# Kernel optimization log

Measured on AMD Instinct MI355X. Metric: run time of the kernel, lower is better.

Reference implementation:

```python
import jax, jax.numpy as jnp
import numpy as np

TEMPERATURE = 0.5
EPS = 1e-8  # torch F.cosine_similarity norm clamp
B, D = 4096, 768


def setup_inputs() -> dict:
    key = jax.random.key(0)
    k1, k2 = jax.random.split(key)
    return {
        "aug_hidden1": jax.random.normal(k1, (B, D), dtype=jnp.float32),
        "aug_hidden2": jax.random.normal(k2, (B, D), dtype=jnp.float32),
    }


def reference(aug_hidden1, aug_hidden2):
    b = aug_hidden1.shape[0]
    n = 2 * b
    h = jnp.concatenate([aug_hidden1, aug_hidden2], axis=0)  # [N, D]
    norm = jnp.maximum(jnp.linalg.norm(h, axis=1, keepdims=True), EPS)
    hn = h / norm
    # cosine-similarity matrix via GEMM (equivalent to broadcasted cosine_similarity)
    sim = jnp.matmul(hn, hn.T) / TEMPERATURE  # [N, N]
    idx = jnp.arange(n)
    pos = sim[idx, (idx + b) % n]  # positives: sim(i, i+B) and sim(i+B, i)
    # row logits = {positive} U {all entries except diagonal and pair} = all off-diagonal
    # entries, so CrossEntropy(label=0) == logsumexp(off-diagonal row) - positive
    sim_masked = jnp.where(jnp.eye(n, dtype=bool), -jnp.inf, sim)
    lse = jax.nn.logsumexp(sim_masked, axis=1)  # [N]
    return jnp.mean(lse - pos)
```

## Files before the change

kernel.cpp:

```cpp
#include <hip/hip_runtime.h>
#include <hip/hip_bf16.h>


#define B_SZ 4096
#define D_SZ 768
#define N_SZ 8192
#define ROWB 384
constexpr float INV_T = 2.0f;

typedef float f32x16 __attribute__((ext_vector_type(16)));
typedef int i32x8 __attribute__((ext_vector_type(8)));
typedef int i32x4 __attribute__((ext_vector_type(4)));
typedef __attribute__((address_space(1))) const unsigned int gu32;
typedef __attribute__((address_space(3))) unsigned int lu32;

__device__ inline void async16(const void* g, void* l) {
    __builtin_amdgcn_global_load_lds((gu32*)g, (lu32*)l, 16, 0, 0);
}

__device__ inline float hsum32_dpp(float x) {
    float s = x, t;
    t = __int_as_float(__builtin_amdgcn_update_dpp(0, __float_as_int(s), 0x111, 0xf, 0xf, true)); s += t;
    t = __int_as_float(__builtin_amdgcn_update_dpp(0, __float_as_int(s), 0x112, 0xf, 0xf, true)); s += t;
    t = __int_as_float(__builtin_amdgcn_update_dpp(0, __float_as_int(s), 0x114, 0xf, 0xf, true)); s += t;
    t = __int_as_float(__builtin_amdgcn_update_dpp(0, __float_as_int(s), 0x118, 0xf, 0xf, true)); s += t;
    t = __int_as_float(__builtin_amdgcn_update_dpp(0, __float_as_int(s), 0x142, 0xa, 0xf, true)); s += t;
    return s;
}

__device__ inline unsigned fp4_enc(float v) {
    float a = fabsf(v);
    unsigned c;
    if (a < 1.25f)      c = (a < 0.25f) ? 0u : (a < 0.75f) ? 1u : 2u;
    else if (a < 2.5f)  c = (a < 1.75f) ? 3u : 4u;
    else                c = (a < 3.5f) ? 5u : (a < 5.0f) ? 6u : 7u;
    return c | (v < 0.f ? 8u : 0u);
}

__global__ __launch_bounds__(256) void prep_k(const float* __restrict__ h1,
                                              const float* __restrict__ h2,
                                              unsigned char* __restrict__ hn4,
                                              float* __restrict__ pos,
                                              float* __restrict__ out) {
    if (blockIdx.x == 0 && threadIdx.x == 0) out[0] = 0.f;
    const int i = blockIdx.x * 4 + (threadIdx.x >> 6);
    const int lane = threadIdx.x & 63;
    const float4* a4 = (const float4*)(h1 + (size_t)i * D_SZ);
    const float4* b4 = (const float4*)(h2 + (size_t)i * D_SZ);
    float4 av[3], bv[3];
    float sa = 0.f, sb = 0.f, dt = 0.f;
#pragma unroll
    for (int j = 0; j < 3; ++j) {
        av[j] = a4[lane * 3 + j];
        bv[j] = b4[lane * 3 + j];
        sa += av[j].x * av[j].x + av[j].y * av[j].y + av[j].z * av[j].z + av[j].w * av[j].w;
        sb += bv[j].x * bv[j].x + bv[j].y * bv[j].y + bv[j].z * bv[j].z + bv[j].w * bv[j].w;
        dt += av[j].x * bv[j].x + av[j].y * bv[j].y + av[j].z * bv[j].z + av[j].w * bv[j].w;
    }
#pragma unroll
    for (int m = 1; m < 64; m <<= 1) {
        sa += __shfl_xor(sa, m, 64);
        sb += __shfl_xor(sb, m, 64);
        dt += __shfl_xor(dt, m, 64);
    }
    const float n1 = fmaxf(sqrtf(sa), 1e-8f), n2 = fmaxf(sqrtf(sb), 1e-8f);
    const float i1 = 1.0f / n1, i2 = 1.0f / n2;
    const float s1 = i1 * 16.0f, s2 = i2 * 16.0f;
    unsigned short* d1 = (unsigned short*)(hn4 + (size_t)i * ROWB);
    unsigned short* d2 = (unsigned short*)(hn4 + (size_t)(i + B_SZ) * ROWB);
#pragma unroll
    for (int j = 0; j < 3; ++j) {
        float va[4] = {av[j].x, av[j].y, av[j].z, av[j].w};
        float vb[4] = {bv[j].x, bv[j].y, bv[j].z, bv[j].w};
        unsigned u1 = 0, u2 = 0;
#pragma unroll
        for (int e = 0; e < 4; ++e) {
            u1 |= fp4_enc(va[e] * s1) << (4 * e);
            u2 |= fp4_enc(vb[e] * s2) << (4 * e);
        }
        d1[lane * 3 + j] = (unsigned short)u1;
        d2[lane * 3 + j] = (unsigned short)u2;
    }
    if (lane == 0) {
        float p = dt * i1 * i2 * INV_T;
        pos[i] = p;
        pos[i + B_SZ] = p;
    }
}

#define BM 128
#define SLAB 4096
#define WINB 64
#define NWIN 6
#define BUFS 8192

__global__ __launch_bounds__(512) void gemm_reduce_k(const unsigned char* __restrict__ hn4,
                                                     float* __restrict__ part) {
    __shared__ __align__(16) unsigned char As[3 * BUFS];
    __shared__ __align__(16) unsigned char Bs[3 * BUFS];
    const int b0 = blockIdx.x;
    const int b = (b0 & 7) * 260 + (b0 >> 3);
    int tx = (int)((sqrtf(8.0f * (float)b + 1.0f) - 1.0f) * 0.5f);
    while ((tx + 1) * (tx + 2) / 2 <= b) ++tx;
    while (tx * (tx + 1) / 2 > b) --tx;
    const int ty = b - tx * (tx + 1) / 2;
    const int rowBase = ty * BM;
    const int colBase = tx * BM;
    const bool diagBlk = (ty == tx);

    const int tid = threadIdx.x;
    const int wave = tid >> 6;
    const int lane = tid & 63;
    const int l32 = lane & 31;
    const int half = lane >> 5;
    const int ms = wave & 3;
    const int nh = wave >> 2;

    f32x16 acc[2];
#pragma unroll
    for (int nt = 0; nt < 2; ++nt)
#pragma unroll
        for (int j = 0; j < 16; ++j) acc[nt][j] = 0.f;

    const bool stB = wave >= 4;
    const int cg = (lane & 1) ^ ((lane >> 3) & 1);
    const unsigned char* gsrc =
        hn4 + (size_t)((stB ? colBase : rowBase) + ms * 32 + (lane >> 1)) * ROWB + cg * 16;
    unsigned char* ldst = (stB ? Bs : As) + ms * 1024;

    const int p = half ^ ((l32 >> 2) & 1);
    const int aOff = (ms * 32 + l32) * 32 + p * 16;
    const int bOff = (nh * 64 + l32) * 32 + p * 16;

    async16(gsrc, ldst);
    async16(gsrc + 32, ldst + SLAB);
    async16(gsrc + WINB, ldst + BUFS);
    async16(gsrc + WINB + 32, ldst + BUFS + SLAB);

#pragma unroll
    for (int w = 0; w < NWIN; ++w) {
        if (w < NWIN - 1) asm volatile("s_waitcnt vmcnt(2)" ::: "memory");
        else              asm volatile("s_waitcnt vmcnt(0)" ::: "memory");
        __builtin_amdgcn_s_barrier();
        __builtin_amdgcn_sched_barrier(0);
        if (w + 2 < NWIN) {
            const unsigned char* g0 = gsrc + (w + 2) * WINB;
            unsigned char* l0 = ldst + ((w + 2) % 3) * BUFS;
            async16(g0, l0);
            async16(g0 + 32, l0 + SLAB);
        }
        const unsigned char* Ab = As + (w % 3) * BUFS;
        const unsigned char* Bb = Bs + (w % 3) * BUFS;
#pragma unroll
        for (int s = 0; s < 2; ++s) {
            i32x4 al = *(const i32x4*)(Ab + s * SLAB + aOff);
            i32x8 a = {al[0], al[1], al[2], al[3], 0, 0, 0, 0};
#pragma unroll
            for (int nt = 0; nt < 2; ++nt) {
                i32x4 bl = *(const i32x4*)(Bb + s * SLAB + bOff + nt * 1024);
                i32x8 bf = {bl[0], bl[1], bl[2], bl[3], 0, 0, 0, 0};
                acc[nt] = __builtin_amdgcn_mfma_scale_f32_32x32x64_f8f6f4(
                    a, bf, acc[nt], 4, 4, 0, 0x7C7C7C7C, 0, 0x7B7B7B7B);
            }
        }
    }
    __syncthreads();

    float* rowS = (float*)As;
    float* colS = (float*)(As + 1024);
    float rs[16];
#pragma unroll
    for (int j = 0; j < 16; ++j) rs[j] = 0.f;
    float csum[2] = {0.f, 0.f};
#pragma unroll
    for (int nt = 0; nt < 2; ++nt) {
        const int col = colBase + nh * 64 + nt * 32 + l32;
#pragma unroll
        for (int j = 0; j < 16; ++j) {
            const int row = rowBase + ms * 32 + (j & 3) + 8 * (j >> 2) + 4 * half;
            float e = __expf(acc[nt][j]);
            e = (diagBlk && row == col) ? 0.f : e;
            rs[j] += e;
            csum[nt] += e;
        }
    }
#pragma unroll
    for (int j = 0; j < 16; ++j) rs[j] = hsum32_dpp(rs[j]);
    if (l32 == 31) {
#pragma unroll
        for (int j = 0; j < 16; ++j)
            rowS[nh * 128 + ms * 32 + (j & 3) + 8 * (j >> 2) + 4 * half] = rs[j];
    }
#pragma unroll
    for (int nt = 0; nt < 2; ++nt) {
        float c = csum[nt] + __shfl_xor(csum[nt], 32, 64);
        if (half == 0) colS[ms * 128 + nh * 64 + nt * 32 + l32] = c;
    }
    __syncthreads();
    if (tid < 128) {
        part[((size_t)ty * 64 + tx) * 128 + tid] = rowS[tid] + rowS[128 + tid];
    } else if (tid < 256 && !diagBlk) {
        const int c = tid - 128;
        part[((size_t)tx * 64 + ty) * 128 + c] =
            colS[c] + colS[128 + c] + colS[256 + c] + colS[384 + c];
    }
}

__global__ __launch_bounds__(128) void finalize_k(const float* __restrict__ part,
                                                  const float* __restrict__ pos,
                                                  float* __restrict__ out) {
    __shared__ float red[2];
    const int t = blockIdx.x;
    const int r = threadIdx.x;
    const float* p = part + (size_t)t * 64 * 128 + r;
    float s = 0.f;
#pragma unroll 16
    for (int u = 0; u < 64; ++u) s += p[u * 128];
    const int i = t * 128 + r;
    float v = __logf(s) - pos[i];
#pragma unroll
    for (int m = 1; m < 64; m <<= 1) v += __shfl_xor(v, m, 64);
    if ((r & 63) == 0) red[r >> 6] = v;
    __syncthreads();
    if (r == 0) atomicAdd(out, (red[0] + red[1]) * (1.0f / (float)N_SZ));
}

extern "C" void kernel_launch(void* const* d_in, const int* in_sizes, int n_in,
                              void* d_out, int out_size, void* d_ws, size_t ws_size,
                              hipStream_t stream) {
    const float* h1 = (const float*)d_in[0];
    const float* h2 = (const float*)d_in[1];
    float* out = (float*)d_out;

    char* ws = (char*)d_ws;
    unsigned char* hn4 = (unsigned char*)ws;
    float* pos  = (float*)(ws + (size_t)N_SZ * ROWB);
    float* part = (float*)(ws + (size_t)N_SZ * ROWB + 32768);

    prep_k<<<B_SZ / 4, 256, 0, stream>>>(h1, h2, hn4, pos, out);
    const int nTiles = N_SZ / BM;
    const int nBlocks = nTiles * (nTiles + 1) / 2;
    gemm_reduce_k<<<nBlocks, 512, 0, stream>>>(hn4, part);
    finalize_k<<<64, 128, 0, stream>>>(part, pos, out);
}
```

Before: 103.0 us.

## Use 4-wave blocks with 2x2 MFMA tiles per wave and double buffering

Shrinks the GEMM-reduce block from 8 to 4 waves. Each wave now computes a 64x64 sub-tile (2x2 MFMA tiles), so every loaded A and B fragment is used twice from registers. Triple-buffered LDS is replaced by double buffering with a full barrier each window, and every wave now loads both A and B slabs. This cuts LDS traffic per MFMA and LDS footprint, which may allow more resident blocks. The cost is less latency hiding, since prefetch is only one window ahead and there are extra barriers, plus higher register pressure from four accumulators.

```diff
diff --git a/kernel.cpp b/kernel.cpp
--- a/kernel.cpp
+++ b/kernel.cpp
@@ -94,10 +94,10 @@
 #define NWIN 6
 #define BUFS 8192
 
-__global__ __launch_bounds__(512) void gemm_reduce_k(const unsigned char* __restrict__ hn4,
+__global__ __launch_bounds__(256) void gemm_reduce_k(const unsigned char* __restrict__ hn4,
                                                      float* __restrict__ part) {
-    __shared__ __align__(16) unsigned char As[3 * BUFS];
-    __shared__ __align__(16) unsigned char Bs[3 * BUFS];
+    __shared__ __align__(16) unsigned char As[2 * BUFS];
+    __shared__ __align__(16) unsigned char Bs[2 * BUFS];
     const int b0 = blockIdx.x;
     const int b = (b0 & 7) * 260 + (b0 >> 3);
     int tx = (int)((sqrtf(8.0f * (float)b + 1.0f) - 1.0f) * 0.5f);
@@ -113,96 +113,116 @@
     const int lane = tid & 63;
     const int l32 = lane & 31;
     const int half = lane >> 5;
-    const int ms = wave & 3;
-    const int nh = wave >> 2;
-
-    f32x16 acc[2];
-#pragma unroll
-    for (int nt = 0; nt < 2; ++nt)
-#pragma unroll
-        for (int j = 0; j < 16; ++j) acc[nt][j] = 0.f;
-
-    const bool stB = wave >= 4;
+    const int wr = wave >> 1;
+    const int wcl = wave & 1;
+
+    f32x16 acc[2][2];
+#pragma unroll
+    for (int mt = 0; mt < 2; ++mt)
+#pragma unroll
+        for (int nt = 0; nt < 2; ++nt)
+#pragma unroll
+            for (int j = 0; j < 16; ++j) acc[mt][nt][j] = 0.f;
+
     const int cg = (lane & 1) ^ ((lane >> 3) & 1);
-    const unsigned char* gsrc =
-        hn4 + (size_t)((stB ? colBase : rowBase) + ms * 32 + (lane >> 1)) * ROWB + cg * 16;
-    unsigned char* ldst = (stB ? Bs : As) + ms * 1024;
+    const unsigned char* gA =
+        hn4 + (size_t)(rowBase + wave * 32 + (lane >> 1)) * ROWB + cg * 16;
+    const unsigned char* gB =
+        hn4 + (size_t)(colBase + wave * 32 + (lane >> 1)) * ROWB + cg * 16;
+    unsigned char* lA = As + wave * 1024;
+    unsigned char* lB = Bs + wave * 1024;
 
     const int p = half ^ ((l32 >> 2) & 1);
-    const int aOff = (ms * 32 + l32) * 32 + p * 16;
-    const int bOff = (nh * 64 + l32) * 32 + p * 16;
-
-    async16(gsrc, ldst);
-    async16(gsrc + 32, ldst + SLAB);
-    async16(gsrc + WINB, ldst + BUFS);
-    async16(gsrc + WINB + 32, ldst + BUFS + SLAB);
-
-#pragma unroll
+    const int aO = wr * 2048 + l32 * 32 + p * 16;
+    const int bO = wcl * 2048 + l32 * 32 + p * 16;
+
+    async16(gA, lA);
+    async16(gA + 32, lA + SLAB);
+    async16(gB, lB);
+    async16(gB + 32, lB + SLAB);
+    __syncthreads();
+
     for (int w = 0; w < NWIN; ++w) {
-        if (w < NWIN - 1) asm volatile("s_waitcnt vmcnt(2)" ::: "memory");
-        else              asm volatile("s_waitcnt vmcnt(0)" ::: "memory");
-        __builtin_amdgcn_s_barrier();
-        __builtin_amdgcn_sched_barrier(0);
-        if (w + 2 < NWIN) {
-            const unsigned char* g0 = gsrc + (w + 2) * WINB;
-            unsigned char* l0 = ldst + ((w + 2) % 3) * BUFS;
-            async16(g0, l0);
-            async16(g0 + 32, l0 + SLAB);
-        }
-        const unsigned char* Ab = As + (w % 3) * BUFS;
-        const unsigned char* Bb = Bs + (w % 3) * BUFS;
+        const int buf = w & 1;
+        if (w + 1 < NWIN) {
+            const int o = (w + 1) * WINB;
+            unsigned char* dA = lA + (buf ^ 1) * BUFS;
+            unsigned char* dB = lB + (buf ^ 1) * BUFS;
+            async16(gA + o, dA);
+            async16(gA + o + 32, dA + SLAB);
+            async16(gB + o, dB);
+            async16(gB + o + 32, dB + SLAB);
+        }
+        const unsigned char* Ab = As + buf * BUFS;
+        const unsigned char* Bb = Bs + buf * BUFS;
 #pragma unroll
         for (int s = 0; s < 2; ++s) {
-            i32x4 al = *(const i32x4*)(Ab + s * SLAB + aOff);
-            i32x8 a = {al[0], al[1], al[2], al[3], 0, 0, 0, 0};
+            i32x8 a[2], bf[2];
+#pragma unroll
+            for (int mt = 0; mt < 2; ++mt) {
+                i32x4 t = *(const i32x4*)(Ab + s * SLAB + aO + mt * 1024);
+                a[mt] = {t[0], t[1], t[2], t[3], 0, 0, 0, 0};
+            }
 #pragma unroll
             for (int nt = 0; nt < 2; ++nt) {
-                i32x4 bl = *(const i32x4*)(Bb + s * SLAB + bOff + nt * 1024);
-                i32x8 bf = {bl[0], bl[1], bl[2], bl[3], 0, 0, 0, 0};
-                acc[nt] = __builtin_amdgcn_mfma_scale_f32_32x32x64_f8f6f4(
-                    a, bf, acc[nt], 4, 4, 0, 0x7C7C7C7C, 0, 0x7B7B7B7B);
+                i32x4 t = *(const i32x4*)(Bb + s * SLAB + bO + nt * 1024);
+                bf[nt] = {t[0], t[1], t[2], t[3], 0, 0, 0, 0};
             }
-        }
-    }
-    __syncthreads();
+#pragma unroll
+            for (int nt = 0; nt < 2; ++nt)
+#pragma unroll
+                for (int mt = 0; mt < 2; ++mt)
+                    acc[mt][nt] = __builtin_amdgcn_mfma_scale_f32_32x32x64_f8f6f4(
+                        a[mt], bf[nt], acc[mt][nt], 4, 4, 0, 0x7C7C7C7C, 0, 0x7B7B7B7B);
+        }
+        __syncthreads();
+    }
 
     float* rowS = (float*)As;
     float* colS = (float*)(As + 1024);
-    float rs[16];
-#pragma unroll
-    for (int j = 0; j < 16; ++j) rs[j] = 0.f;
+    float rs[2][16];
+#pragma unroll
+    for (int mt = 0; mt < 2; ++mt)
+#pragma unroll
+        for (int j = 0; j < 16; ++j) rs[mt][j] = 0.f;
     float csum[2] = {0.f, 0.f};
 #pragma unroll
-    for (int nt = 0; nt < 2; ++nt) {
-        const int col = colBase + nh * 64 + nt * 32 + l32;
-#pragma unroll
-        for (int j = 0; j < 16; ++j) {
-            const int row = rowBase + ms * 32 + (j & 3) + 8 * (j >> 2) + 4 * half;
-            float e = __expf(acc[nt][j]);
-            e = (diagBlk && row == col) ? 0.f : e;
-            rs[j] += e;
-            csum[nt] += e;
-        }
-    }
-#pragma unroll
-    for (int j = 0; j < 16; ++j) rs[j] = hsum32_dpp(rs[j]);
+    for (int mt = 0; mt < 2; ++mt)
+#pragma unroll
+        for (int nt = 0; nt < 2; ++nt) {
+            const int col = colBase + wcl * 64 + nt * 32 + l32;
+#pragma unroll
+            for (int j = 0; j < 16; ++j) {
+                const int row = rowBase + wr * 64 + mt * 32 + (j & 3) + 8 * (j >> 2) + 4 * half;
+                float e = __expf(acc[mt][nt][j]);
+                e = (diagBlk && row == col) ? 0.f : e;
+                rs[mt][j] += e;
+                csum[nt] += e;
+            }
+        }
+#pragma unroll
+    for (int mt = 0; mt < 2; ++mt)
+#pragma unroll
+        for (int j = 0; j < 16; ++j) rs[mt][j] = hsum32_dpp(rs[mt][j]);
     if (l32 == 31) {
 #pragma unroll
-        for (int j = 0; j < 16; ++j)
-            rowS[nh * 128 + ms * 32 + (j & 3) + 8 * (j >> 2) + 4 * half] = rs[j];
+        for (int mt = 0; mt < 2; ++mt)
+#pragma unroll
+            for (int j = 0; j < 16; ++j)
+                rowS[wcl * 128 + wr * 64 + mt * 32 + (j & 3) + 8 * (j >> 2) + 4 * half] =
+                    rs[mt][j];
     }
 #pragma unroll
     for (int nt = 0; nt < 2; ++nt) {
         float c = csum[nt] + __shfl_xor(csum[nt], 32, 64);
-        if (half == 0) colS[ms * 128 + nh * 64 + nt * 32 + l32] = c;
+        if (half == 0) colS[wr * 128 + wcl * 64 + nt * 32 + l32] = c;
     }
     __syncthreads();
     if (tid < 128) {
         part[((size_t)ty * 64 + tx) * 128 + tid] = rowS[tid] + rowS[128 + tid];
-    } else if (tid < 256 && !diagBlk) {
+    } else if (!diagBlk) {
         const int c = tid - 128;
-        part[((size_t)tx * 64 + ty) * 128 + c] =
-            colS[c] + colS[128 + c] + colS[256 + c] + colS[384 + c];
+        part[((size_t)tx * 64 + ty) * 128 + c] = colS[c] + colS[128 + c];
     }
 }
 
@@ -240,6 +260,6 @@
     prep_k<<<B_SZ / 4, 256, 0, stream>>>(h1, h2, hn4, pos, out);
     const int nTiles = N_SZ / BM;
     const int nBlocks = nTiles * (nTiles + 1) / 2;
-    gemm_reduce_k<<<nBlocks, 512, 0, stream>>>(hn4, part);
+    gemm_reduce_k<<<nBlocks, 256, 0, stream>>>(hn4, part);
     finalize_k<<<64, 128, 0, stream>>>(part, pos, out);
 }
```

Measured after the change: 129.9 us. 26.0% more time.

## Load MFMA operands directly from global memory instead of staging through LDS

Applied to the files above, without the earlier changes.

Removes the triple-buffered async global-to-LDS staging with its barriers, so each wave now reads its FP4 A and B fragments straight from global memory with one-step register prefetching. The goal is to drop LDS traffic and barrier synchronisation in a short K loop of 12 slabs. The cost is that A fragments are fetched redundantly by both wave halves and B fragments by all four row waves, so L2/global traffic rises. Latency hiding now relies on a single prefetch step rather than a deeper pipeline.

```diff
diff --git a/kernel.cpp b/kernel.cpp
--- a/kernel.cpp
+++ b/kernel.cpp
@@ -6,17 +6,12 @@
 #define D_SZ 768
 #define N_SZ 8192
 #define ROWB 384
+#define NSLAB 12
 constexpr float INV_T = 2.0f;
 
 typedef float f32x16 __attribute__((ext_vector_type(16)));
 typedef int i32x8 __attribute__((ext_vector_type(8)));
 typedef int i32x4 __attribute__((ext_vector_type(4)));
-typedef __attribute__((address_space(1))) const unsigned int gu32;
-typedef __attribute__((address_space(3))) unsigned int lu32;
-
-__device__ inline void async16(const void* g, void* l) {
-    __builtin_amdgcn_global_load_lds((gu32*)g, (lu32*)l, 16, 0, 0);
-}
 
 __device__ inline float hsum32_dpp(float x) {
     float s = x, t;
@@ -89,15 +84,11 @@
 }
 
 #define BM 128
-#define SLAB 4096
-#define WINB 64
-#define NWIN 6
-#define BUFS 8192
 
 __global__ __launch_bounds__(512) void gemm_reduce_k(const unsigned char* __restrict__ hn4,
                                                      float* __restrict__ part) {
-    __shared__ __align__(16) unsigned char As[3 * BUFS];
-    __shared__ __align__(16) unsigned char Bs[3 * BUFS];
+    __shared__ float rowS[256];
+    __shared__ float colS[512];
     const int b0 = blockIdx.x;
     const int b = (b0 & 7) * 260 + (b0 >> 3);
     int tx = (int)((sqrtf(8.0f * (float)b + 1.0f) - 1.0f) * 0.5f);
@@ -122,52 +113,33 @@
 #pragma unroll
         for (int j = 0; j < 16; ++j) acc[nt][j] = 0.f;
 
-    const bool stB = wave >= 4;
-    const int cg = (lane & 1) ^ ((lane >> 3) & 1);
-    const unsigned char* gsrc =
-        hn4 + (size_t)((stB ? colBase : rowBase) + ms * 32 + (lane >> 1)) * ROWB + cg * 16;
-    unsigned char* ldst = (stB ? Bs : As) + ms * 1024;
-
-    const int p = half ^ ((l32 >> 2) & 1);
-    const int aOff = (ms * 32 + l32) * 32 + p * 16;
-    const int bOff = (nh * 64 + l32) * 32 + p * 16;
-
-    async16(gsrc, ldst);
-    async16(gsrc + 32, ldst + SLAB);
-    async16(gsrc + WINB, ldst + BUFS);
-    async16(gsrc + WINB + 32, ldst + BUFS + SLAB);
-
-#pragma unroll
-    for (int w = 0; w < NWIN; ++w) {
-        if (w < NWIN - 1) asm volatile("s_waitcnt vmcnt(2)" ::: "memory");
-        else              asm volatile("s_waitcnt vmcnt(0)" ::: "memory");
-        __builtin_amdgcn_s_barrier();
-        __builtin_amdgcn_sched_barrier(0);
-        if (w + 2 < NWIN) {
-            const unsigned char* g0 = gsrc + (w + 2) * WINB;
-            unsigned char* l0 = ldst + ((w + 2) % 3) * BUFS;
-            async16(g0, l0);
-            async16(g0 + 32, l0 + SLAB);
+    const unsigned char* pa =
+        hn4 + (size_t)(rowBase + ms * 32 + l32) * ROWB + half * 16;
+    const unsigned char* pb0 =
+        hn4 + (size_t)(colBase + nh * 64 + l32) * ROWB + half * 16;
+    const unsigned char* pb1 = pb0 + 32 * ROWB;
+
+    i32x4 ac = *(const i32x4*)pa;
+    i32x4 b0c = *(const i32x4*)pb0;
+    i32x4 b1c = *(const i32x4*)pb1;
+    for (int t = 0; t < NSLAB; ++t) {
+        i32x4 an, b0n, b1n;
+        if (t + 1 < NSLAB) {
+            const int o = (t + 1) * 32;
+            an  = *(const i32x4*)(pa + o);
+            b0n = *(const i32x4*)(pb0 + o);
+            b1n = *(const i32x4*)(pb1 + o);
         }
-        const unsigned char* Ab = As + (w % 3) * BUFS;
-        const unsigned char* Bb = Bs + (w % 3) * BUFS;
-#pragma unroll
-        for (int s = 0; s < 2; ++s) {
-            i32x4 al = *(const i32x4*)(Ab + s * SLAB + aOff);
-            i32x8 a = {al[0], al[1], al[2], al[3], 0, 0, 0, 0};
-#pragma unroll
-            for (int nt = 0; nt < 2; ++nt) {
-                i32x4 bl = *(const i32x4*)(Bb + s * SLAB + bOff + nt * 1024);
-                i32x8 bf = {bl[0], bl[1], bl[2], bl[3], 0, 0, 0, 0};
-                acc[nt] = __builtin_amdgcn_mfma_scale_f32_32x32x64_f8f6f4(
-                    a, bf, acc[nt], 4, 4, 0, 0x7C7C7C7C, 0, 0x7B7B7B7B);
-            }
-        }
-    }
-    __syncthreads();
-
-    float* rowS = (float*)As;
-    float* colS = (float*)(As + 1024);
+        i32x8 a  = {ac[0], ac[1], ac[2], ac[3], 0, 0, 0, 0};
+        i32x8 v0 = {b0c[0], b0c[1], b0c[2], b0c[3], 0, 0, 0, 0};
+        i32x8 v1 = {b1c[0], b1c[1], b1c[2], b1c[3], 0, 0, 0, 0};
+        acc[0] = __builtin_amdgcn_mfma_scale_f32_32x32x64_f8f6f4(
+            a, v0, acc[0], 4, 4, 0, 0x7C7C7C7C, 0, 0x7B7B7B7B);
+        acc[1] = __builtin_amdgcn_mfma_scale_f32_32x32x64_f8f6f4(
+            a, v1, acc[1], 4, 4, 0, 0x7C7C7C7C, 0, 0x7B7B7B7B);
+        ac = an; b0c = b0n; b1c = b1n;
+    }
+
     float rs[16];
 #pragma unroll
     for (int j = 0; j < 16; ++j) rs[j] = 0.f;
```

New measurement: 150.0 us. 45.6% more time.

## Load A operand directly to registers and double-buffer only B in LDS

Applied to the files above, without the earlier changes.

The A (row) operand is no longer staged through shared memory. Each wave loads its A fragments straight from global memory into registers and prefetches the next window one step ahead. Only B is staged in LDS, using a 2-deep double buffer instead of the 3-deep triple buffer for both operands. This roughly halves LDS use and removes the A LDS round trip, which could raise occupancy. The cost is a full __syncthreads per window, a shallower prefetch, and redundant global reads of A across waves that share a row slice (both column halves).

```diff
diff --git a/kernel.cpp b/kernel.cpp
--- a/kernel.cpp
+++ b/kernel.cpp
@@ -96,8 +96,7 @@
 
 __global__ __launch_bounds__(512) void gemm_reduce_k(const unsigned char* __restrict__ hn4,
                                                      float* __restrict__ part) {
-    __shared__ __align__(16) unsigned char As[3 * BUFS];
-    __shared__ __align__(16) unsigned char Bs[3 * BUFS];
+    __shared__ __align__(16) unsigned char Bs[2 * BUFS];
     const int b0 = blockIdx.x;
     const int b = (b0 & 7) * 260 + (b0 >> 3);
     int tx = (int)((sqrtf(8.0f * (float)b + 1.0f) - 1.0f) * 0.5f);
@@ -122,52 +121,53 @@
 #pragma unroll
         for (int j = 0; j < 16; ++j) acc[nt][j] = 0.f;
 
-    const bool stB = wave >= 4;
+    const int sSt = wave & 1;
+    const int rb = (wave >> 1) * 32;
     const int cg = (lane & 1) ^ ((lane >> 3) & 1);
-    const unsigned char* gsrc =
-        hn4 + (size_t)((stB ? colBase : rowBase) + ms * 32 + (lane >> 1)) * ROWB + cg * 16;
-    unsigned char* ldst = (stB ? Bs : As) + ms * 1024;
+    const unsigned char* gB =
+        hn4 + (size_t)(colBase + rb + (lane >> 1)) * ROWB + sSt * 32 + cg * 16;
+    unsigned char* lB = Bs + sSt * SLAB + rb * 32;
+
+    const unsigned char* pa =
+        hn4 + (size_t)(rowBase + ms * 32 + l32) * ROWB + half * 16;
 
     const int p = half ^ ((l32 >> 2) & 1);
-    const int aOff = (ms * 32 + l32) * 32 + p * 16;
-    const int bOff = (nh * 64 + l32) * 32 + p * 16;
-
-    async16(gsrc, ldst);
-    async16(gsrc + 32, ldst + SLAB);
-    async16(gsrc + WINB, ldst + BUFS);
-    async16(gsrc + WINB + 32, ldst + BUFS + SLAB);
-
-#pragma unroll
+    const int bO = (nh * 64 + l32) * 32 + p * 16;
+
+    async16(gB, lB);
+    i32x4 aCur[2];
+    aCur[0] = *(const i32x4*)pa;
+    aCur[1] = *(const i32x4*)(pa + 32);
+    __syncthreads();
+
     for (int w = 0; w < NWIN; ++w) {
-        if (w < NWIN - 1) asm volatile("s_waitcnt vmcnt(2)" ::: "memory");
-        else              asm volatile("s_waitcnt vmcnt(0)" ::: "memory");
-        __builtin_amdgcn_s_barrier();
-        __builtin_amdgcn_sched_barrier(0);
-        if (w + 2 < NWIN) {
-            const unsigned char* g0 = gsrc + (w + 2) * WINB;
-            unsigned char* l0 = ldst + ((w + 2) % 3) * BUFS;
-            async16(g0, l0);
-            async16(g0 + 32, l0 + SLAB);
-        }
-        const unsigned char* Ab = As + (w % 3) * BUFS;
-        const unsigned char* Bb = Bs + (w % 3) * BUFS;
+        const int buf = w & 1;
+        i32x4 aNxt[2];
+        if (w + 1 < NWIN) {
+            const int o = (w + 1) * WINB;
+            async16(gB + o, lB + (buf ^ 1) * BUFS);
+            aNxt[0] = *(const i32x4*)(pa + o);
+            aNxt[1] = *(const i32x4*)(pa + o + 32);
+        }
+        const unsigned char* Bb = Bs + buf * BUFS;
 #pragma unroll
         for (int s = 0; s < 2; ++s) {
-            i32x4 al = *(const i32x4*)(Ab + s * SLAB + aOff);
-            i32x8 a = {al[0], al[1], al[2], al[3], 0, 0, 0, 0};
+            i32x8 a = {aCur[s][0], aCur[s][1], aCur[s][2], aCur[s][3], 0, 0, 0, 0};
 #pragma unroll
             for (int nt = 0; nt < 2; ++nt) {
-                i32x4 bl = *(const i32x4*)(Bb + s * SLAB + bOff + nt * 1024);
+                i32x4 bl = *(const i32x4*)(Bb + s * SLAB + bO + nt * 1024);
                 i32x8 bf = {bl[0], bl[1], bl[2], bl[3], 0, 0, 0, 0};
                 acc[nt] = __builtin_amdgcn_mfma_scale_f32_32x32x64_f8f6f4(
                     a, bf, acc[nt], 4, 4, 0, 0x7C7C7C7C, 0, 0x7B7B7B7B);
             }
         }
-    }
-    __syncthreads();
-
-    float* rowS = (float*)As;
-    float* colS = (float*)(As + 1024);
+        __syncthreads();
+        aCur[0] = aNxt[0];
+        aCur[1] = aNxt[1];
+    }
+
+    float* rowS = (float*)Bs;
+    float* colS = (float*)(Bs + 1024);
     float rs[16];
 #pragma unroll
     for (int j = 0; j < 16; ++j) rs[j] = 0.f;
```

After: 112.5 us. 1.09x slower.
